# Kernel optimization log

Hardware: AMD Instinct MI355X
Metric: run time of the kernel (lower is better)

Reference implementation:

```python
import jax, jax.numpy as jnp
import numpy as np

B, T, H, NH, HD = 2, 2048, 2048, 16, 128


def setup_inputs() -> dict:
    key = jax.random.key(0)
    k1, k2, k3 = jax.random.split(key, 3)
    hidden_states = jax.random.normal(k1, (B, T, H), dtype=jnp.float32)
    w_qkv = jax.random.normal(k2, (3 * H, H), dtype=jnp.float32) * (1.0 / np.sqrt(H))
    w_out = jax.random.normal(k3, (H, H), dtype=jnp.float32) * (1.0 / np.sqrt(H))
    return {"hidden_states": hidden_states, "w_qkv": w_qkv, "w_out": w_out}


def reference(hidden_states, w_qkv, w_out):
    scale = 1.0 / np.sqrt(HD)
    # qkv projection: torch Linear is x @ W.T with W [out, in]
    qkv = jnp.einsum('bth,oh->bto', hidden_states, w_qkv)  # [B, T, 3H]
    q, k, v = jnp.split(qkv, 3, axis=2)
    # [B, NH, T, HD]
    q = q.reshape(B, T, NH, HD).transpose(0, 2, 1, 3)
    k = k.reshape(B, T, NH, HD).transpose(0, 2, 1, 3)
    v = v.reshape(B, T, NH, HD).transpose(0, 2, 1, 3)
    scores = jnp.einsum('bhqd,bhkd->bhqk', q, k) * scale  # [B, NH, T, T]
    mask = jnp.tril(jnp.ones((T, T), dtype=bool))  # causal
    scores = jnp.where(mask[None, None], scores, -jnp.inf)
    probs = jax.nn.softmax(scores, axis=-1)
    attn = jnp.einsum('bhqk,bhkd->bhqd', probs, v)  # [B, NH, T, HD]
    attn = attn.transpose(0, 2, 1, 3).reshape(B, T, H)
    out = jnp.einsum('bth,oh->bto', attn, w_out)
    return out
```

## Files before the change

kernel.cpp:

```cpp
#include <hip/hip_runtime.h>
#include <cstdint>
#include <cstddef>

typedef _Float16 f16x8 __attribute__((ext_vector_type(8)));
typedef _Float16 f16x4 __attribute__((ext_vector_type(4)));
typedef float    f32x4 __attribute__((ext_vector_type(4)));
typedef unsigned short ushort_t;

#define LOG2E 1.4426950408889634f

constexpr int BATCH = 2;
constexpr int TSEQ  = 2048;
constexpr int HID   = 2048;
constexpr int NH    = 16;
constexpr int HD    = 128;
constexpr int GK    = 2048;
constexpr int NKT   = GK / 64;

__device__ inline f32x4 mfma16(f16x8 a, f16x8 b, f32x4 c) {
    return __builtin_amdgcn_mfma_f32_16x16x32_f16(a, b, c, 0, 0, 0);
}

__device__ inline void async_copy16(const void* src, void* dst_lds) {
    __builtin_amdgcn_global_load_lds(
        (const __attribute__((address_space(1))) uint32_t*)src,
        (__attribute__((address_space(3))) uint32_t*)dst_lds, 16, 0, 0);
}

__global__ __launch_bounds__(256)
void cast_all(const float4* __restrict__ hs, const float4* __restrict__ wqkv,
              const float4* __restrict__ wout, f16x4* __restrict__ hs_h,
              f16x4* __restrict__ wqkv_h, f16x4* __restrict__ wout_h,
              int n_hs, int n_wqkv, int n_wout) {
    int i = blockIdx.x * 256 + threadIdx.x;
    const float4* src; f16x4* dst; int j;
    if (i < n_hs)                 { src = hs;   dst = hs_h;   j = i; }
    else if (i < n_hs + n_wqkv)   { src = wqkv; dst = wqkv_h; j = i - n_hs; }
    else if (i < n_hs + n_wqkv + n_wout) { src = wout; dst = wout_h; j = i - n_hs - n_wqkv; }
    else return;
    float4 v = src[j];
    f16x4 o = { (_Float16)v.x, (_Float16)v.y, (_Float16)v.z, (_Float16)v.w };
    dst[j] = o;
}

template <int MODE>
__global__ __launch_bounds__(512, 2)
void gemm_big(const _Float16* __restrict__ A, const _Float16* __restrict__ B,
              float* __restrict__ C, _Float16* __restrict__ Qo,
              _Float16* __restrict__ Ko, _Float16* __restrict__ Vo, int NB) {
    __shared__ __align__(16) _Float16 As[3][256 * 64];
    __shared__ __align__(16) _Float16 Bs[3][128 * 64];

    const int tid  = threadIdx.x;
    const int lane = tid & 63;
    const int w    = tid >> 6;
    const int l15  = lane & 15;
    const int lq   = lane >> 4;
    const int wr   = w >> 1, wc = w & 1;

    const int bid = (int)blockIdx.x;
    const int cpx = (int)gridDim.x >> 3;
    const int swz = (bid & 7) * cpx + (bid >> 3);
    const int bn  = swz % NB, bm = swz / NB;
    const int m0  = bm * 256, n0 = bn * 128;

    const _Float16* Ab = A + (size_t)m0 * GK;
    const _Float16* Bb = B + (size_t)n0 * GK;

    auto stage = [&](int t, int b) {
        const int k0 = t * 64;
        #pragma unroll
        for (int it = 0; it < 4; ++it) {
            const int slot = it * 512 + tid;
            const int row = slot >> 3, c16 = slot & 7;
            const int srcb = c16 ^ (row & 7);
            async_copy16(Ab + (size_t)row * GK + k0 + srcb * 8,
                         (char*)As[b] + slot * 16);
        }
        #pragma unroll
        for (int it = 0; it < 2; ++it) {
            const int slot = it * 512 + tid;
            const int row = slot >> 3, c16 = slot & 7;
            const int srcb = c16 ^ (row & 7);
            async_copy16(Bb + (size_t)row * GK + k0 + srcb * 8,
                         (char*)Bs[b] + slot * 16);
        }
    };

    f32x4 acc[4][4] = {};

    stage(0, 0);
    stage(1, 1);

    for (int t = 0; t < NKT; ++t) {
        if (t + 1 < NKT) asm volatile("s_waitcnt vmcnt(6)" ::: "memory");
        else             asm volatile("s_waitcnt vmcnt(0)" ::: "memory");
        __builtin_amdgcn_s_barrier();
        __builtin_amdgcn_sched_barrier(0);

        const char* At_ = (const char*)As[t % 3];
        const char* Bt_ = (const char*)Bs[t % 3];

        f16x8 af[4][2], bff[4][2];
        #pragma unroll
        for (int i = 0; i < 4; ++i)
            #pragma unroll
            for (int kk = 0; kk < 2; ++kk) {
                const int ra = wr * 64 + i * 16 + l15;
                af[i][kk]  = *(const f16x8*)(At_ + ra * 128 + (((kk * 4 + lq) ^ (ra & 7)) << 4));
                const int rb = wc * 64 + i * 16 + l15;
                bff[i][kk] = *(const f16x8*)(Bt_ + rb * 128 + (((kk * 4 + lq) ^ (rb & 7)) << 4));
            }

        if (t + 2 < NKT) stage(t + 2, (t + 2) % 3);

        __builtin_amdgcn_s_setprio(1);
        #pragma unroll
        for (int kk = 0; kk < 2; ++kk)
            #pragma unroll
            for (int i = 0; i < 4; ++i)
                #pragma unroll
                for (int j = 0; j < 4; ++j)
                    acc[i][j] = mfma16(af[i][kk], bff[j][kk], acc[i][j]);
        __builtin_amdgcn_s_setprio(0);
    }

    if (MODE == 0) {
        #pragma unroll
        for (int j = 0; j < 4; ++j) {
            const int ncol = n0 + wc * 64 + j * 16 + l15;
            const int which = ncol >> 11;
            const int oo = ncol & 2047;
            const int head = oo >> 7;
            const int d = oo & 127;
            _Float16* dst = (which == 0) ? Qo : (which == 1) ? Ko : Vo;
            const float scl = (which == 0) ? 0.08838834764831845f : 1.0f;
            #pragma unroll
            for (int i = 0; i < 4; ++i) {
                #pragma unroll
                for (int r = 0; r < 4; ++r) {
                    const int m = m0 + wr * 64 + i * 16 + lq * 4 + r;
                    const int b = m >> 11, tt = m & 2047;
                    dst[((size_t)(b * NH + head) * TSEQ + tt) * HD + d] =
                        (_Float16)(acc[i][j][r] * scl);
                }
            }
        }
    } else {
        #pragma unroll
        for (int i = 0; i < 4; ++i)
            #pragma unroll
            for (int j = 0; j < 4; ++j)
                #pragma unroll
                for (int r = 0; r < 4; ++r) {
                    const int m = m0 + wr * 64 + i * 16 + lq * 4 + r;
                    const int n = n0 + wc * 64 + j * 16 + l15;
                    C[(size_t)m * HID + n] = acc[i][j][r];
                }
    }
}

template <int MODE>
__global__ __launch_bounds__(256, 2)
void gemm_small(const _Float16* __restrict__ A, const _Float16* __restrict__ B,
                float* __restrict__ C, int NB) {
    __shared__ __align__(16) _Float16 As[2][128 * 64];
    __shared__ __align__(16) _Float16 Bs[2][128 * 64];

    const int tid  = threadIdx.x;
    const int lane = tid & 63;
    const int w    = tid >> 6;
    const int l15  = lane & 15;
    const int lq   = lane >> 4;
    const int wr   = w >> 1, wc = w & 1;

    const int bid = (int)blockIdx.x;
    const int cpx = (int)gridDim.x >> 3;
    const int swz = (bid & 7) * cpx + (bid >> 3);
    const int bn  = swz % NB, bm = swz / NB;
    const int m0  = bm * 128, n0 = bn * 128;

    const _Float16* Ab = A + (size_t)m0 * GK;
    const _Float16* Bb = B + (size_t)n0 * GK;

    auto stage = [&](int t, int b) {
        const int k0 = t * 64;
        #pragma unroll
        for (int it = 0; it < 4; ++it) {
            const int slot = it * 256 + tid;
            const int row = slot >> 3, c16 = slot & 7;
            const int srcb = c16 ^ (row & 7);
            async_copy16(Ab + (size_t)row * GK + k0 + srcb * 8,
                         (char*)As[b] + slot * 16);
        }
        #pragma unroll
        for (int it = 0; it < 4; ++it) {
            const int slot = it * 256 + tid;
            const int row = slot >> 3, c16 = slot & 7;
            const int srcb = c16 ^ (row & 7);
            async_copy16(Bb + (size_t)row * GK + k0 + srcb * 8,
                         (char*)Bs[b] + slot * 16);
        }
    };

    f32x4 acc[4][4] = {};

    stage(0, 0);
    stage(1, 1);

    for (int t = 0; t < NKT; ++t) {
        const int cur = t & 1;
        if (t + 1 < NKT) asm volatile("s_waitcnt vmcnt(8)" ::: "memory");
        else             asm volatile("s_waitcnt vmcnt(0)" ::: "memory");
        __builtin_amdgcn_s_barrier();
        __builtin_amdgcn_sched_barrier(0);

        const char* At_ = (const char*)As[cur];
        const char* Bt_ = (const char*)Bs[cur];

        f16x8 af[4][2], bff[4][2];
        #pragma unroll
        for (int i = 0; i < 4; ++i)
            #pragma unroll
            for (int kk = 0; kk < 2; ++kk) {
                const int ra = wr * 64 + i * 16 + l15;
                af[i][kk]  = *(const f16x8*)(At_ + ra * 128 + (((kk * 4 + lq) ^ (ra & 7)) << 4));
                const int rb = wc * 64 + i * 16 + l15;
                bff[i][kk] = *(const f16x8*)(Bt_ + rb * 128 + (((kk * 4 + lq) ^ (rb & 7)) << 4));
            }
        asm volatile("s_waitcnt lgkmcnt(0)" ::: "memory");
        __builtin_amdgcn_sched_barrier(0);
        __builtin_amdgcn_s_barrier();
        __builtin_amdgcn_sched_barrier(0);

        if (t + 2 < NKT) stage(t + 2, cur);

        __builtin_amdgcn_s_setprio(1);
        #pragma unroll
        for (int kk = 0; kk < 2; ++kk)
            #pragma unroll
            for (int i = 0; i < 4; ++i)
                #pragma unroll
                for (int j = 0; j < 4; ++j)
                    acc[i][j] = mfma16(af[i][kk], bff[j][kk], acc[i][j]);
        __builtin_amdgcn_s_setprio(0);
    }

    #pragma unroll
    for (int i = 0; i < 4; ++i)
        #pragma unroll
        for (int j = 0; j < 4; ++j)
            #pragma unroll
            for (int r = 0; r < 4; ++r) {
                const int m = m0 + wr * 64 + i * 16 + lq * 4 + r;
                const int n = n0 + wc * 64 + j * 16 + l15;
                C[(size_t)m * HID + n] = acc[i][j][r];
            }
}

__global__ __launch_bounds__(256)
void attn_fwd(const _Float16* __restrict__ Q, const _Float16* __restrict__ K,
              const _Float16* __restrict__ V, _Float16* __restrict__ O) {
    __shared__ __align__(16) char Ks[64 * 256];
    __shared__ __align__(16) char Vt[128 * 128];
    __shared__ __align__(16) char Ps[4][2048];

    const int tid  = threadIdx.x;
    const int lane = tid & 63;
    const int w    = tid >> 6;
    const int l15  = lane & 15;
    const int lq   = lane >> 4;

    const int bh   = (int)blockIdx.x & 31;
    const int pair = (int)blockIdx.x >> 5;
    const int b = bh >> 4, h = bh & 15;

    const size_t base = (size_t)bh * TSEQ * HD;
    const _Float16* Qp = Q + base;
    const _Float16* Kp = K + base;
    const _Float16* Vp = V + base;

    const f16x8 ones = { (_Float16)1.f, (_Float16)1.f, (_Float16)1.f, (_Float16)1.f,
                         (_Float16)1.f, (_Float16)1.f, (_Float16)1.f, (_Float16)1.f };

    uint4 vv[4];
    auto loadV = [&](int t) {
        const int row = tid & 63;
        #pragma unroll
        for (int it = 0; it < 4; ++it) {
            const int c8 = w * 4 + it;
            vv[it] = *(const uint4*)(Vp + (size_t)(t * 64 + row) * HD + c8 * 8);
        }
    };
    auto stageK = [&](int t) {
        #pragma unroll
        for (int it = 0; it < 4; ++it) {
            const int slot = it * 256 + tid;
            const int row = slot >> 4, c16 = slot & 15;
            const int srcb = c16 ^ (row & 7);
            async_copy16(Kp + (size_t)(t * 64 + row) * HD + srcb * 8, Ks + slot * 16);
        }
    };
    auto writeV = [&]() {
        const int row = tid & 63;
        #pragma unroll
        for (int it = 0; it < 4; ++it) {
            const int c8 = w * 4 + it;
            const uint32_t wrd[4] = {vv[it].x, vv[it].y, vv[it].z, vv[it].w};
            #pragma unroll
            for (int p2 = 0; p2 < 4; ++p2) {
                const int d0 = c8 * 8 + p2 * 2, d1 = d0 + 1;
                int b0 = d0 * 128 + row * 2; b0 ^= (d0 & 7) << 4;
                int b1 = d1 * 128 + row * 2; b1 ^= (d1 & 7) << 4;
                *(ushort_t*)(Vt + b0) = (ushort_t)(wrd[p2] & 0xffffu);
                *(ushort_t*)(Vt + b1) = (ushort_t)(wrd[p2] >> 16);
            }
        }
    };

    char* Pb = Ps[w];

    for (int phase = 0; phase < 2; ++phase) {
        const int qt = phase ? pair : (31 - pair);
        const int q0 = qt * 64;
        const int NT = qt + 1;

        if (phase) __syncthreads();

        const int qrow = q0 + w * 16 + l15;
        f16x8 qf[4];
        #pragma unroll
        for (int ks = 0; ks < 4; ++ks)
            qf[ks] = *(const f16x8*)(Qp + (size_t)qrow * HD + ks * 32 + lq * 8);

        f32x4 o[8] = {};
        f32x4 osum = {};
        float m_run[4];
        #pragma unroll
        for (int r = 0; r < 4; ++r) m_run[r] = -1e30f;

        stageK(0);
        loadV(0);

        for (int t = 0; t < NT; ++t) {
            writeV();
            __syncthreads();
            if (t + 1 < NT) loadV(t + 1);

            const int kv0 = t * 64;
            f32x4 s[4] = {};
            __builtin_amdgcn_s_setprio(1);
            #pragma unroll
            for (int ks = 0; ks < 4; ++ks) {
                #pragma unroll
                for (int nf = 0; nf < 4; ++nf) {
                    const int r   = nf * 16 + l15;
                    const int blk = (ks * 4 + lq) ^ (r & 7);
                    const f16x8 kf = *(const f16x8*)(Ks + r * 256 + blk * 16);
                    s[nf] = mfma16(qf[ks], kf, s[nf]);
                }
            }
            __builtin_amdgcn_s_setprio(0);

            if (kv0 + 63 > q0 + w * 16) {
                #pragma unroll
                for (int nf = 0; nf < 4; ++nf) {
                    const int kvp = kv0 + nf * 16 + l15;
                    #pragma unroll
                    for (int r = 0; r < 4; ++r)
                        if (kvp > q0 + w * 16 + lq * 4 + r) s[nf][r] = -1e30f;
                }
            }

            bool need = false;
            #pragma unroll
            for (int r = 0; r < 4; ++r) {
                const float v = fmaxf(fmaxf(s[0][r], s[1][r]), fmaxf(s[2][r], s[3][r]));
                need = need || (v > m_run[r] + 5.0f);
            }
            if (__any(need)) {
                float alpha[4];
                #pragma unroll
                for (int r = 0; r < 4; ++r) {
                    float v = fmaxf(fmaxf(s[0][r], s[1][r]), fmaxf(s[2][r], s[3][r]));
                    v = fmaxf(v, __shfl_xor(v, 1));
                    v = fmaxf(v, __shfl_xor(v, 2));
                    v = fmaxf(v, __shfl_xor(v, 4));
                    v = fmaxf(v, __shfl_xor(v, 8));
                    const float mn = fmaxf(m_run[r], v);
                    alpha[r] = __builtin_exp2f((m_run[r] - mn) * LOG2E);
                    m_run[r] = mn;
                }
                #pragma unroll
                for (int df = 0; df < 8; ++df)
                    #pragma unroll
                    for (int r = 0; r < 4; ++r)
                        o[df][r] *= alpha[r];
                #pragma unroll
                for (int r = 0; r < 4; ++r) osum[r] *= alpha[r];
            }

            #pragma unroll
            for (int nf = 0; nf < 4; ++nf) {
                #pragma unroll
                for (int r = 0; r < 4; ++r) {
                    const float p = __builtin_exp2f((s[nf][r] - m_run[r]) * LOG2E);
                    const int qp = lq * 4 + r;
                    int byt = qp * 128 + (nf * 16 + l15) * 2;
                    byt ^= (qp & 7) << 4;
                    union { _Float16 hf; ushort_t u; } cv;
                    cv.hf = (_Float16)p;
                    *(ushort_t*)(Pb + byt) = cv.u;
                }
            }

            __builtin_amdgcn_s_setprio(1);
            #pragma unroll
            for (int ks2 = 0; ks2 < 2; ++ks2) {
                const int pblk = (ks2 * 4 + lq) ^ (l15 & 7);
                const f16x8 pf = *(const f16x8*)(Pb + l15 * 128 + pblk * 16);
                #pragma unroll
                for (int df = 0; df < 8; ++df) {
                    const int vr   = df * 16 + l15;
                    const int vblk = (ks2 * 4 + lq) ^ (vr & 7);
                    const f16x8 vf = *(const f16x8*)(Vt + vr * 128 + vblk * 16);
                    o[df] = mfma16(pf, vf, o[df]);
                }
                osum = mfma16(pf, ones, osum);
            }
            __builtin_amdgcn_s_setprio(0);

            if (t + 1 < NT) {
                __syncthreads();
                stageK(t + 1);
            }
        }

        float rl[4];
        #pragma unroll
        for (int r = 0; r < 4; ++r) rl[r] = 1.0f / osum[r];
        #pragma unroll
        for (int df = 0; df < 8; ++df) {
            #pragma unroll
            for (int r = 0; r < 4; ++r) {
                const int qg = q0 + w * 16 + lq * 4 + r;
                const int dg = df * 16 + l15;
                O[((size_t)(b * TSEQ + qg)) * HID + h * HD + dg] =
                    (_Float16)(o[df][r] * rl[r]);
            }
        }
    }
}

extern "C" void kernel_launch(void* const* d_in, const int* in_sizes, int n_in,
                              void* d_out, int out_size, void* d_ws, size_t ws_size,
                              hipStream_t stream) {
    (void)in_sizes; (void)n_in; (void)out_size; (void)ws_size;
    const float* hs   = (const float*)d_in[0];
    const float* wqkv = (const float*)d_in[1];
    const float* wout = (const float*)d_in[2];

    char* ws = (char*)d_ws;
    size_t off = 0;
    _Float16* hs_h   = (_Float16*)(ws + off); off += (size_t)BATCH * TSEQ * HID * 2;
    _Float16* wqkv_h = (_Float16*)(ws + off); off += (size_t)3 * HID * HID * 2;
    _Float16* wout_h = (_Float16*)(ws + off); off += (size_t)HID * HID * 2;
    _Float16* Qh     = (_Float16*)(ws + off); off += (size_t)BATCH * NH * TSEQ * HD * 2;
    _Float16* Kh     = (_Float16*)(ws + off); off += (size_t)BATCH * NH * TSEQ * HD * 2;
    _Float16* Vh     = (_Float16*)(ws + off); off += (size_t)BATCH * NH * TSEQ * HD * 2;
    _Float16* At     = (_Float16*)(ws + off); off += (size_t)BATCH * TSEQ * HID * 2;

    const int n4_hs   = BATCH * TSEQ * HID / 4;
    const int n4_wqkv = 3 * HID * HID / 4;
    const int n4_wout = HID * HID / 4;
    const int n4_all  = n4_hs + n4_wqkv + n4_wout;
    cast_all<<<dim3((n4_all + 255) / 256), dim3(256), 0, stream>>>(
        (const float4*)hs, (const float4*)wqkv, (const float4*)wout,
        (f16x4*)hs_h, (f16x4*)wqkv_h, (f16x4*)wout_h, n4_hs, n4_wqkv, n4_wout);

    gemm_big<0><<<dim3(768), dim3(512), 0, stream>>>(
        hs_h, wqkv_h, nullptr, Qh, Kh, Vh, 48);

    attn_fwd<<<dim3(512), dim3(256), 0, stream>>>(Qh, Kh, Vh, At);

    gemm_small<1><<<dim3(512), dim3(256), 0, stream>>>(
        At, wout_h, (float*)d_out, 16);
}
```

Before: 262.9 us.

## Compute transposed S tile and pass P through registers instead of LDS

The QK^T MFMA operands are swapped so each lane holds one query row's scores across KV positions. That reduces the softmax max to a single per-lane value with two cross-lane shuffles. P is now packed to fp16 pairs with cvt_pkrtz and redistributed into the PV MFMA operand layout using ds_bpermute shuffles instead of a per-wave LDS round-trip. The row sum is accumulated in scalar registers rather than through an extra MFMA with a ones vector. This cuts LDS traffic and MFMA count, at the cost of more shuffle instructions and round-toward-zero conversion of P.

After: 263.5 us, median of 3. About the same (+0.3%).

```diff
diff --git a/kernel.cpp b/kernel.cpp
--- a/kernel.cpp
+++ b/kernel.cpp
@@ -25,6 +25,12 @@
     __builtin_amdgcn_global_load_lds(
         (const __attribute__((address_space(1))) uint32_t*)src,
         (__attribute__((address_space(3))) uint32_t*)dst_lds, 16, 0, 0);
+}
+
+__device__ inline uint32_t pkrtz(float a, float b) {
+    union { decltype(__builtin_amdgcn_cvt_pkrtz(0.f, 0.f)) h; uint32_t u; } cv;
+    cv.h = __builtin_amdgcn_cvt_pkrtz(a, b);
+    return cv.u;
 }
 
 __global__ __launch_bounds__(256)
@@ -263,13 +269,15 @@
               const _Float16* __restrict__ V, _Float16* __restrict__ O) {
     __shared__ __align__(16) char Ks[64 * 256];
     __shared__ __align__(16) char Vt[128 * 128];
-    __shared__ __align__(16) char Ps[4][2048];
 
     const int tid  = threadIdx.x;
     const int lane = tid & 63;
     const int w    = tid >> 6;
     const int l15  = lane & 15;
     const int lq   = lane >> 4;
+    const int lq1  = lq >> 1;
+    const int laneA = l15 + ((lane & 16) << 1);
+    const int laneB = laneA + 16;
 
     const int bh   = (int)blockIdx.x & 31;
     const int pair = (int)blockIdx.x >> 5;
@@ -279,9 +287,6 @@
     const _Float16* Qp = Q + base;
     const _Float16* Kp = K + base;
     const _Float16* Vp = V + base;
-
-    const f16x8 ones = { (_Float16)1.f, (_Float16)1.f, (_Float16)1.f, (_Float16)1.f,
-                         (_Float16)1.f, (_Float16)1.f, (_Float16)1.f, (_Float16)1.f };
 
     uint4 vv[4];
     auto loadV = [&](int t) {
@@ -318,8 +323,6 @@
         }
     };
 
-    char* Pb = Ps[w];
-
     for (int phase = 0; phase < 2; ++phase) {
         const int qt = phase ? pair : (31 - pair);
         const int q0 = qt * 64;
@@ -334,10 +337,8 @@
             qf[ks] = *(const f16x8*)(Qp + (size_t)qrow * HD + ks * 32 + lq * 8);
 
         f32x4 o[8] = {};
-        f32x4 osum = {};
-        float m_run[4];
-        #pragma unroll
-        for (int r = 0; r < 4; ++r) m_run[r] = -1e30f;
+        float m_run = -1e30f;
+        float osum  = 0.0f;
 
         stageK(0);
         loadV(0);
@@ -357,76 +358,90 @@
                     const int r   = nf * 16 + l15;
                     const int blk = (ks * 4 + lq) ^ (r & 7);
                     const f16x8 kf = *(const f16x8*)(Ks + r * 256 + blk * 16);
-                    s[nf] = mfma16(qf[ks], kf, s[nf]);
+                    s[nf] = mfma16(kf, qf[ks], s[nf]);
                 }
             }
             __builtin_amdgcn_s_setprio(0);
 
             if (kv0 + 63 > q0 + w * 16) {
+                const int q_lane = q0 + w * 16 + l15;
                 #pragma unroll
                 for (int nf = 0; nf < 4; ++nf) {
-                    const int kvp = kv0 + nf * 16 + l15;
                     #pragma unroll
-                    for (int r = 0; r < 4; ++r)
-                        if (kvp > q0 + w * 16 + lq * 4 + r) s[nf][r] = -1e30f;
+                    for (int r = 0; r < 4; ++r) {
+                        const int kv = kv0 + nf * 16 + lq * 4 + r;
+                        if (kv > q_lane) s[nf][r] = -1e30f;
+                    }
                 }
             }
 
-            bool need = false;
-            #pragma unroll
-            for (int r = 0; r < 4; ++r) {
-                const float v = fmaxf(fmaxf(s[0][r], s[1][r]), fmaxf(s[2][r], s[3][r]));
-                need = need || (v > m_run[r] + 5.0f);
-            }
-            if (__any(need)) {
-                float alpha[4];
-                #pragma unroll
-                for (int r = 0; r < 4; ++r) {
-                    float v = fmaxf(fmaxf(s[0][r], s[1][r]), fmaxf(s[2][r], s[3][r]));
-                    v = fmaxf(v, __shfl_xor(v, 1));
-                    v = fmaxf(v, __shfl_xor(v, 2));
-                    v = fmaxf(v, __shfl_xor(v, 4));
-                    v = fmaxf(v, __shfl_xor(v, 8));
-                    const float mn = fmaxf(m_run[r], v);
-                    alpha[r] = __builtin_exp2f((m_run[r] - mn) * LOG2E);
-                    m_run[r] = mn;
-                }
+            float lmax = -1e30f;
+            #pragma unroll
+            for (int nf = 0; nf < 4; ++nf)
+                lmax = fmaxf(lmax, fmaxf(fmaxf(s[nf][0], s[nf][1]),
+                                         fmaxf(s[nf][2], s[nf][3])));
+            if (__any(lmax > m_run + 5.0f)) {
+                float v = lmax;
+                v = fmaxf(v, __shfl_xor(v, 16));
+                v = fmaxf(v, __shfl_xor(v, 32));
+                const float mn = fmaxf(m_run, v);
+                const float alpha = __builtin_exp2f((m_run - mn) * LOG2E);
+                m_run = mn;
+                osum *= alpha;
+                float aq[4];
+                #pragma unroll
+                for (int r = 0; r < 4; ++r)
+                    aq[r] = __shfl(alpha, lq * 4 + r);
                 #pragma unroll
                 for (int df = 0; df < 8; ++df)
                     #pragma unroll
                     for (int r = 0; r < 4; ++r)
-                        o[df][r] *= alpha[r];
-                #pragma unroll
-                for (int r = 0; r < 4; ++r) osum[r] *= alpha[r];
-            }
-
+                        o[df][r] *= aq[r];
+            }
+
+            uint32_t pk[4][2];
+            float psum = 0.0f;
             #pragma unroll
             for (int nf = 0; nf < 4; ++nf) {
                 #pragma unroll
-                for (int r = 0; r < 4; ++r) {
-                    const float p = __builtin_exp2f((s[nf][r] - m_run[r]) * LOG2E);
-                    const int qp = lq * 4 + r;
-                    int byt = qp * 128 + (nf * 16 + l15) * 2;
-                    byt ^= (qp & 7) << 4;
-                    union { _Float16 hf; ushort_t u; } cv;
-                    cv.hf = (_Float16)p;
-                    *(ushort_t*)(Pb + byt) = cv.u;
+                for (int hh = 0; hh < 2; ++hh) {
+                    const float pa = __builtin_exp2f((s[nf][2 * hh]     - m_run) * LOG2E);
+                    const float pb = __builtin_exp2f((s[nf][2 * hh + 1] - m_run) * LOG2E);
+                    psum += pa + pb;
+                    pk[nf][hh] = pkrtz(pa, pb);
                 }
             }
+            osum += psum;
+
+            f16x8 pf[2];
+            #pragma unroll
+            for (int ks2 = 0; ks2 < 2; ++ks2) {
+                union { uint32_t u[4]; f16x8 v; } pu;
+                const uint32_t a0n0 = (uint32_t)__shfl((int)pk[2 * ks2][0],     laneA);
+                const uint32_t a0n1 = (uint32_t)__shfl((int)pk[2 * ks2 + 1][0], laneA);
+                const uint32_t a1n0 = (uint32_t)__shfl((int)pk[2 * ks2][1],     laneA);
+                const uint32_t a1n1 = (uint32_t)__shfl((int)pk[2 * ks2 + 1][1], laneA);
+                const uint32_t b0n0 = (uint32_t)__shfl((int)pk[2 * ks2][0],     laneB);
+                const uint32_t b0n1 = (uint32_t)__shfl((int)pk[2 * ks2 + 1][0], laneB);
+                const uint32_t b1n0 = (uint32_t)__shfl((int)pk[2 * ks2][1],     laneB);
+                const uint32_t b1n1 = (uint32_t)__shfl((int)pk[2 * ks2 + 1][1], laneB);
+                pu.u[0] = lq1 ? a0n1 : a0n0;
+                pu.u[1] = lq1 ? a1n1 : a1n0;
+                pu.u[2] = lq1 ? b0n1 : b0n0;
+                pu.u[3] = lq1 ? b1n1 : b1n0;
+                pf[ks2] = pu.v;
+            }
 
             __builtin_amdgcn_s_setprio(1);
             #pragma unroll
             for (int ks2 = 0; ks2 < 2; ++ks2) {
-                const int pblk = (ks2 * 4 + lq) ^ (l15 & 7);
-                const f16x8 pf = *(const f16x8*)(Pb + l15 * 128 + pblk * 16);
                 #pragma unroll
                 for (int df = 0; df < 8; ++df) {
                     const int vr   = df * 16 + l15;
                     const int vblk = (ks2 * 4 + lq) ^ (vr & 7);
                     const f16x8 vf = *(const f16x8*)(Vt + vr * 128 + vblk * 16);
-                    o[df] = mfma16(pf, vf, o[df]);
+                    o[df] = mfma16(pf[ks2], vf, o[df]);
                 }
-                osum = mfma16(pf, ones, osum);
             }
             __builtin_amdgcn_s_setprio(0);
 
@@ -436,9 +451,15 @@
             }
         }
 
-        float rl[4];
-        #pragma unroll
-        for (int r = 0; r < 4; ++r) rl[r] = 1.0f / osum[r];
+        float tot = osum;
+        tot += __shfl_xor(tot, 16);
+        tot += __shfl_xor(tot, 32);
+        const float rl = 1.0f / tot;
+        float rlq[4];
+        #pragma unroll
+        for (int r = 0; r < 4; ++r)
+            rlq[r] = __shfl(rl, lq * 4 + r);
+
         #pragma unroll
         for (int df = 0; df < 8; ++df) {
             #pragma unroll
@@ -446,7 +467,7 @@
                 const int qg = q0 + w * 16 + lq * 4 + r;
                 const int dg = df * 16 + l15;
                 O[((size_t)(b * TSEQ + qg)) * HID + h * HD + dg] =
-                    (_Float16)(o[df][r] * rl[r]);
+                    (_Float16)(o[df][r] * rlq[r]);
             }
         }
     }
```
